# Kernel tuning notes

Hardware: AMD Instinct MI355X
Metric: run time of the kernel (lower is better)

The kernel has to match this reference:

```python
import jax, jax.numpy as jnp
import numpy as np

B, T, C = 4, 2048, 1024
H, HS = 16, 64


def setup_inputs() -> dict:
    key = jax.random.key(0)
    ks = jax.random.split(key, 5)
    scale = (H * C) ** (-0.5)
    x = jax.random.normal(ks[0], (B, T, C), dtype=jnp.float32)
    Wk = jax.random.normal(ks[1], (H, C, HS), dtype=jnp.float32) * scale
    Wq = jax.random.normal(ks[2], (H, C, HS), dtype=jnp.float32) * scale
    Wv = jax.random.normal(ks[3], (H, C, HS), dtype=jnp.float32) * scale
    proj_w = jax.random.normal(ks[4], (C, C), dtype=jnp.float32) / C ** 0.5
    proj_b = jnp.zeros((C,), dtype=jnp.float32)
    return {"x": x, "Wk": Wk, "Wq": Wq, "Wv": Wv, "proj_w": proj_w, "proj_b": proj_b}


def reference(x, Wk, Wq, Wv, proj_w, proj_b):
    b, t, c = x.shape
    # per-head projections: (B,T,C) x (H,C,D) -> (B,H,T,D)
    q = jnp.einsum('btc,hcd->bhtd', x, Wq)
    k = jnp.einsum('btc,hcd->bhtd', x, Wk)
    v = jnp.einsum('btc,hcd->bhtd', x, Wv)
    # NOTE: original module does not scale by 1/sqrt(head_size)
    wei = jnp.einsum('bhtd,bhsd->bhts', q, k)  # (B,H,T,T)
    causal = jnp.tril(jnp.ones((t, t), dtype=bool))
    wei = jnp.where(causal, wei, -jnp.inf)
    wei = jax.nn.softmax(wei, axis=-1)
    out = jnp.einsum('bhts,bhsd->bhtd', wei, v)
    out = out.transpose(0, 2, 1, 3).reshape(b, t, c)  # concat heads
    return out @ proj_w + proj_b
```

## Files before the change

### kernel.cpp

```cpp
#include <hip/hip_runtime.h>

typedef unsigned short u16;
typedef u16 u16x4 __attribute__((ext_vector_type(4)));
typedef u16 u16x8 __attribute__((ext_vector_type(8)));
typedef unsigned uint2v __attribute__((ext_vector_type(2)));
typedef unsigned uint4v __attribute__((ext_vector_type(4)));
typedef __bf16 bf16x2 __attribute__((ext_vector_type(2)));
typedef __bf16 bf16x8 __attribute__((ext_vector_type(8)));
typedef float f32x4 __attribute__((ext_vector_type(4)));

#define DEV static __device__ __forceinline__

DEV u16 f2bf(float f) {
  union { float f; unsigned u; } v; v.f = f;
  return (u16)((v.u + 0x7FFFu + ((v.u >> 16) & 1u)) >> 16);
}

DEV void async16(const void* g, void* l) {
  __builtin_amdgcn_global_load_lds((const __attribute__((address_space(1))) void*)g,
                                   (__attribute__((address_space(3))) void*)l, 16, 0, 0);
}

DEV f32x4 mfma16(bf16x8 a, bf16x8 b, f32x4 c) {
  return __builtin_amdgcn_mfma_f32_16x16x32_bf16(a, b, c, 0, 0, 0);
}

DEV float exp2fast(float x) { return __builtin_amdgcn_exp2f(x); }

#define BARRIER() asm volatile("s_barrier" ::: "memory")
#define SB0() __builtin_amdgcn_sched_barrier(0)

__global__ __launch_bounds__(256) void k_prep(const float* __restrict__ x,
                                              const float* __restrict__ Wk,
                                              const float* __restrict__ Wq,
                                              const float* __restrict__ Wv,
                                              const float* __restrict__ pw,
                                              u16* __restrict__ xb,
                                              u16* __restrict__ wT,
                                              u16* __restrict__ pwT) {
  __shared__ float t[64 * 72];
  const int bid = blockIdx.x, tid = threadIdx.x;
  if (bid < 8192) {
    int i = bid * 1024 + tid * 4;
    float4 v = *(const float4*)(x + i);
    u16x4 o = { f2bf(v.x), f2bf(v.y), f2bf(v.z), f2bf(v.w) };
    *(u16x4*)(xb + i) = o;
    return;
  }
  const int role = bid - 8192;
  const float* src;
  u16* dst;
  int rows, cols, bx, by, bz;
  float scale;
  if (role < 768) {
    const int w = role >> 8, rem = role & 255;
    src = (w == 0) ? Wq : ((w == 1) ? Wk : Wv);
    dst = wT + (size_t)w * 1024 * 1024;
    scale = (w == 0) ? 1.44269504088896340736f : 1.0f;
    rows = 1024; cols = 64; bx = 0; by = rem >> 4; bz = rem & 15;
  } else {
    const int p = role - 768;
    src = pw; dst = pwT; scale = 1.0f;
    rows = 1024; cols = 1024; bx = p & 15; by = p >> 4; bz = 0;
  }
  src += (size_t)bz * rows * cols;
  dst += (size_t)bz * rows * cols;
  const int c0 = bx * 64, r0 = by * 64;
  const int rr = tid >> 2, cb = (tid & 3) * 16;
  const float* s = src + (size_t)(r0 + rr) * cols + c0 + cb;
  float4 v0 = *(const float4*)(s + 0);
  float4 v1 = *(const float4*)(s + 4);
  float4 v2 = *(const float4*)(s + 8);
  float4 v3 = *(const float4*)(s + 12);
  *(float4*)(t + rr * 72 + cb + 0)  = v0;
  *(float4*)(t + rr * 72 + cb + 4)  = v1;
  *(float4*)(t + rr * 72 + cb + 8)  = v2;
  *(float4*)(t + rr * 72 + cb + 12) = v3;
  __syncthreads();
  const int dd = tid >> 2, eb = (tid & 3) * 16;
  u16x8 o0, o1;
#pragma unroll
  for (int e = 0; e < 8; ++e) o0[e] = f2bf(t[(eb + e) * 72 + dd] * scale);
#pragma unroll
  for (int e = 0; e < 8; ++e) o1[e] = f2bf(t[(eb + 8 + e) * 72 + dd] * scale);
  u16* dp = dst + (size_t)(c0 + dd) * rows + r0 + eb;
  *(u16x8*)dp = o0;
  *(u16x8*)(dp + 8) = o1;
}

template <int MODE>
__global__ __launch_bounds__(512, 2) void k_gemm(const u16* __restrict__ A,
                                                 const u16* __restrict__ Bt,
                                                 u16* __restrict__ qd,
                                                 u16* __restrict__ kd,
                                                 u16* __restrict__ vd,
                                                 float* __restrict__ out,
                                                 const float* __restrict__ bias) {
  __shared__ u16 lds[3 * 24576];
  const int tid = threadIdx.x;
  const int w = tid >> 6, lane = tid & 63;
  const int quad = lane >> 4, l15 = lane & 15;
  const int wm = w >> 1, wn = w & 1;

  const int gx = (int)gridDim.x;
  int lin = (int)blockIdx.y * gx + (int)blockIdx.x;
  const int nwg = gx * (int)gridDim.y;
  lin = (lin & 7) * (nwg >> 3) + (lin >> 3);
  const size_t mb = (size_t)(lin / gx);
  const int nb = lin % gx;

  const int lr = lane >> 3;
  const int lc = ((lane & 7) ^ lr) << 3;
  const u16* ga0 = A  + (mb * 256 + (size_t)(w * 8 + lr)) * 1024 + lc;
  const u16* gb0 = Bt + ((size_t)nb * 128 + (size_t)(w * 8 + lr)) * 1024 + lc;

  const int swz0 = ((0 + quad) ^ (l15 & 7)) << 3;
  const int swz1 = ((4 + quad) ^ (l15 & 7)) << 3;

  f32x4 acc[4][4] = {};

#pragma unroll
  for (int s2 = 0; s2 < 2; ++s2) {
    u16* d = lds + s2 * 24576 + w * 512;
#pragma unroll
    for (int g = 0; g < 4; ++g) async16(ga0 + (size_t)g * 65536 + s2 * 64, d + g * 4096);
#pragma unroll
    for (int g = 0; g < 2; ++g) async16(gb0 + (size_t)g * 65536 + s2 * 64, d + 16384 + g * 4096);
  }
  asm volatile("s_waitcnt vmcnt(6)" ::: "memory");
  BARRIER(); SB0();

#pragma unroll
  for (int s = 0; s < 16; ++s) {
    const u16* Ab = lds + (s % 3) * 24576;
    const u16* Bb = Ab + 16384;

    bf16x8 a0[4], b0[4];
#pragma unroll
    for (int i = 0; i < 4; ++i)
      a0[i] = *(const bf16x8*)(Ab + (wm * 64 + i * 16 + l15) * 64 + swz0);
#pragma unroll
    for (int j = 0; j < 4; ++j)
      b0[j] = *(const bf16x8*)(Bb + (wn * 64 + j * 16 + l15) * 64 + swz0);
    if (s < 14) {
      u16* d = lds + ((s + 2) % 3) * 24576 + w * 512;
      async16(ga0 + 0 * 65536 + (s + 2) * 64, d + 0 * 4096);
      async16(ga0 + 1 * 65536 + (s + 2) * 64, d + 1 * 4096);
      async16(ga0 + 2 * 65536 + (s + 2) * 64, d + 2 * 4096);
    }
    SB0(); BARRIER(); SB0();
    __builtin_amdgcn_s_setprio(1);
#pragma unroll
    for (int i = 0; i < 4; ++i)
#pragma unroll
      for (int j = 0; j < 4; ++j) acc[i][j] = mfma16(a0[i], b0[j], acc[i][j]);
    __builtin_amdgcn_s_setprio(0);
    SB0(); BARRIER(); SB0();

    bf16x8 a1[4], b1[4];
#pragma unroll
    for (int i = 0; i < 4; ++i)
      a1[i] = *(const bf16x8*)(Ab + (wm * 64 + i * 16 + l15) * 64 + swz1);
#pragma unroll
    for (int j = 0; j < 4; ++j)
      b1[j] = *(const bf16x8*)(Bb + (wn * 64 + j * 16 + l15) * 64 + swz1);
    if (s < 14) {
      u16* d = lds + ((s + 2) % 3) * 24576 + w * 512;
      async16(ga0 + 3 * 65536 + (s + 2) * 64, d + 3 * 4096);
      async16(gb0 + 0 * 65536 + (s + 2) * 64, d + 16384 + 0 * 4096);
      async16(gb0 + 1 * 65536 + (s + 2) * 64, d + 16384 + 4096);
    }
    SB0(); BARRIER(); SB0();
    __builtin_amdgcn_s_setprio(1);
#pragma unroll
    for (int i = 0; i < 4; ++i)
#pragma unroll
      for (int j = 0; j < 4; ++j) acc[i][j] = mfma16(a1[i], b1[j], acc[i][j]);
    __builtin_amdgcn_s_setprio(0);
    SB0();
    if (s < 14)       { asm volatile("s_waitcnt vmcnt(6)" ::: "memory"); }
    else if (s == 14) { asm volatile("s_waitcnt vmcnt(0)" ::: "memory"); }
    if (s < 15) { BARRIER(); SB0(); }
  }

  const size_t m0 = mb * 256 + wm * 64;
  const int n0 = nb * 128 + wn * 64;
  if (MODE == 0) {
#pragma unroll
    for (int j = 0; j < 4; ++j) {
      const int n = n0 + j * 16 + l15;
      const int p = n >> 10, hh = (n >> 6) & 15, d = n & 63;
      if (p == 2) {
#pragma unroll
        for (int i = 0; i < 4; ++i) {
          const size_t m = m0 + i * 16 + quad * 4;
          const size_t bb = m >> 11, tt = m & 2047;
          u16x4 pk = { f2bf(acc[i][j][0]), f2bf(acc[i][j][1]),
                       f2bf(acc[i][j][2]), f2bf(acc[i][j][3]) };
          *(u16x4*)(vd + ((bb * 16 + hh) * 64 + d) * 2048 + tt) = pk;
        }
      } else {
        u16* dst = (p == 0) ? qd : kd;
#pragma unroll
        for (int i = 0; i < 4; ++i)
#pragma unroll
          for (int r = 0; r < 4; ++r) {
            const size_t m = m0 + i * 16 + quad * 4 + r;
            const size_t bb = m >> 11, tt = m & 2047;
            dst[((bb * 16 + hh) * 2048 + tt) * 64 + d] = f2bf(acc[i][j][r]);
          }
      }
    }
  } else {
#pragma unroll
    for (int j = 0; j < 4; ++j) {
      const int n = n0 + j * 16 + l15;
      const float bv = bias[n];
#pragma unroll
      for (int i = 0; i < 4; ++i)
#pragma unroll
        for (int r = 0; r < 4; ++r) {
          const size_t m = m0 + i * 16 + quad * 4 + r;
          out[m * 1024 + n] = acc[i][j][r] + bv;
        }
    }
  }
}

__global__ __launch_bounds__(256) void k_attn(const u16* __restrict__ Qg,
                                              const u16* __restrict__ Kg,
                                              const u16* __restrict__ Vtg,
                                              u16* __restrict__ Og) {
  __shared__ u16 Kbuf[2 * 4096];
  __shared__ u16 Vbuf[2 * 4096];
  const int tid = threadIdx.x;
  const int wave = tid >> 6, lane = tid & 63;
  const int quad = lane >> 4, l15 = lane & 15;
  const int quad4 = quad * 4, quad8 = quad * 8;
  const int bh = blockIdx.x;
  const int qb = 15 - (int)blockIdx.y;
  const u16* kg = Kg + (size_t)bh * 2048 * 64;
  const u16* vg = Vtg + (size_t)bh * 64 * 2048;
  const int b = bh >> 4, h = bh & 15;

  const int lrow = lane >> 3;
  const int lchunk = ((lane & 7) ^ lrow) << 3;
  const u16* kst = kg + (size_t)(wave * 16 + lrow) * 64 + lchunk;
  const u16* vst = vg + (size_t)(wave * 16 + lrow) * 2048 + lchunk;
  u16* kdst0 = Kbuf + wave * 1024;
  u16* vdst0 = Vbuf + wave * 1024;

  const int rowoff = l15 * 64;
  const int swz0 = ((0 + quad) ^ (l15 & 7)) << 3;
  const int swz1 = ((4 + quad) ^ (l15 & 7)) << 3;

  const int qlo = qb * 128 + wave * 32;
  const int ntw = 2 * qb + 1 + (wave >> 1);
  const int ntb = 2 * qb + 2;
  const u16* qg = Qg + ((size_t)bh * 2048 + (size_t)qb * 128) * 64;

  bf16x8 qf[2][2];
#pragma unroll
  for (int i = 0; i < 2; ++i)
#pragma unroll
    for (int c = 0; c < 2; ++c)
      qf[i][c] = *(const bf16x8*)(qg + (size_t)(wave * 32 + i * 16 + l15) * 64 +
                                  c * 32 + quad8);

  f32x4 oacc[2][4] = {};
  f32x4 lacc[2] = {};
  const f32x4 fzero = {};
  const u16x8 onesu = {0x3F80, 0x3F80, 0x3F80, 0x3F80,
                       0x3F80, 0x3F80, 0x3F80, 0x3F80};
  const bf16x8 onesf = __builtin_bit_cast(bf16x8, onesu);

  async16(kst, kdst0);
  async16(kst + 512, kdst0 + 512);
  async16(vst, vdst0);
  async16(vst + 16384, vdst0 + 512);

  for (int it = 0; it < ntb; ++it) {
    __syncthreads();

    if (it + 1 < ntb) {
      const int buf = (it + 1) & 1;
      const size_t s0n = (size_t)(it + 1) * 64;
      async16(kst + s0n * 64,       kdst0 + buf * 4096);
      async16(kst + s0n * 64 + 512, kdst0 + buf * 4096 + 512);
      async16(vst + s0n,            vdst0 + buf * 4096);
      async16(vst + s0n + 16384,    vdst0 + buf * 4096 + 512);
    }

    if (it < ntw) {
      const int s0 = it * 64;
      const u16* Kb = Kbuf + (it & 1) * 4096;
      const u16* Vb = Vbuf + (it & 1) * 4096;

      f32x4 sacc[4][2];
      __builtin_amdgcn_s_setprio(1);
#pragma unroll
      for (int j = 0; j < 4; ++j) {
        bf16x8 kf0 = *(const bf16x8*)(Kb + j * 1024 + rowoff + swz0);
        bf16x8 kf1 = *(const bf16x8*)(Kb + j * 1024 + rowoff + swz1);
        sacc[j][0] = mfma16(kf0, qf[0][0], fzero);
        sacc[j][0] = mfma16(kf1, qf[0][1], sacc[j][0]);
        sacc[j][1] = mfma16(kf0, qf[1][0], fzero);
        sacc[j][1] = mfma16(kf1, qf[1][1], sacc[j][1]);
      }
      __builtin_amdgcn_s_setprio(0);

#pragma unroll
      for (int j = 0; j < 4; ++j)
#pragma unroll
        for (int i = 0; i < 2; ++i)
#pragma unroll
          for (int r = 0; r < 4; ++r)
            sacc[j][i][r] = exp2fast(sacc[j][i][r]);

      if (it == ntw - 1) {
#pragma unroll
        for (int j = 0; j < 4; ++j)
#pragma unroll
          for (int i = 0; i < 2; ++i)
#pragma unroll
            for (int r = 0; r < 4; ++r)
              if (s0 + j * 16 + quad4 + r > qlo + i * 16 + l15) sacc[j][i][r] = 0.f;
      }

      bf16x8 pa[2][2];
#pragma unroll
      for (int i = 0; i < 2; ++i) {
        unsigned P[8];
#pragma unroll
        for (int j = 0; j < 4; ++j) {
          bf16x2 lo = { (__bf16)sacc[j][i][0], (__bf16)sacc[j][i][1] };
          bf16x2 hi = { (__bf16)sacc[j][i][2], (__bf16)sacc[j][i][3] };
          P[j * 2 + 0] = __builtin_bit_cast(unsigned, lo);
          P[j * 2 + 1] = __builtin_bit_cast(unsigned, hi);
        }
        unsigned wd[8];
#pragma unroll
        for (int g = 0; g < 4; ++g) {
          const int x = (g & 2) * 2 + (g & 1);
          uint2v t = __builtin_amdgcn_permlane32_swap(P[x], P[x + 2], false, false);
          uint2v u = __builtin_amdgcn_permlane16_swap(t.x, t.y, false, false);
          wd[x] = u.x;
          wd[x + 2] = u.y;
        }
        uint4v lo4 = { wd[0], wd[1], wd[2], wd[3] };
        uint4v hi4 = { wd[4], wd[5], wd[6], wd[7] };
        pa[i][0] = __builtin_bit_cast(bf16x8, lo4);
        pa[i][1] = __builtin_bit_cast(bf16x8, hi4);
      }

      __builtin_amdgcn_s_setprio(1);
#pragma unroll
      for (int n = 0; n < 4; ++n) {
        bf16x8 vf0 = *(const bf16x8*)(Vb + n * 1024 + rowoff + swz0);
        bf16x8 vf1 = *(const bf16x8*)(Vb + n * 1024 + rowoff + swz1);
        oacc[0][n] = mfma16(pa[0][0], vf0, oacc[0][n]);
        oacc[0][n] = mfma16(pa[0][1], vf1, oacc[0][n]);
        oacc[1][n] = mfma16(pa[1][0], vf0, oacc[1][n]);
        oacc[1][n] = mfma16(pa[1][1], vf1, oacc[1][n]);
      }
      lacc[0] = mfma16(pa[0][0], onesf, lacc[0]);
      lacc[0] = mfma16(pa[0][1], onesf, lacc[0]);
      lacc[1] = mfma16(pa[1][0], onesf, lacc[1]);
      lacc[1] = mfma16(pa[1][1], onesf, lacc[1]);
      __builtin_amdgcn_s_setprio(0);
    }
  }

#pragma unroll
  for (int i = 0; i < 2; ++i)
#pragma unroll
    for (int r = 0; r < 4; ++r) {
      const float inv = 1.0f / lacc[i][r];
      const size_t t = (size_t)qb * 128 + wave * 32 + i * 16 + quad4 + r;
#pragma unroll
      for (int n = 0; n < 4; ++n)
        Og[((size_t)b * 2048 + t) * 1024 + h * 64 + n * 16 + l15] =
            f2bf(oacc[i][n][r] * inv);
    }
}

extern "C" void kernel_launch(void* const* d_in, const int* in_sizes, int n_in,
                              void* d_out, int out_size, void* d_ws, size_t ws_size,
                              hipStream_t stream) {
  const float* x  = (const float*)d_in[0];
  const float* Wk = (const float*)d_in[1];
  const float* Wq = (const float*)d_in[2];
  const float* Wv = (const float*)d_in[3];
  const float* pw = (const float*)d_in[4];
  const float* pb = (const float*)d_in[5];
  float* out = (float*)d_out;
  char* ws = (char*)d_ws;

  u16* xb  = (u16*)(ws + 0);
  u16* wT  = (u16*)(ws + 16777216);
  u16* pwT = (u16*)(ws + 23068672);
  u16* q   = (u16*)(ws + 25165824);
  u16* kb  = (u16*)(ws + 41943040);
  u16* vt  = (u16*)(ws + 58720256);
  u16* att = (u16*)(ws + 0);

  k_prep<<<9216, 256, 0, stream>>>(x, Wk, Wq, Wv, pw, xb, wT, pwT);
  k_gemm<0><<<dim3(24, 32), 512, 0, stream>>>(xb, wT, q, kb, vt, nullptr, nullptr);
  k_attn<<<dim3(64, 16), 256, 0, stream>>>(q, kb, vt, att);
  k_gemm<1><<<dim3(8, 32), 512, 0, stream>>>(att, pwT, nullptr, nullptr, nullptr, out, pb);
}
```

Measured before the change: 235.1 us.

## Widen QKV GEMM tile to 256 columns and simplify to double-buffered pipeline

```diff
diff --git a/kernel.cpp b/kernel.cpp
--- a/kernel.cpp
+++ b/kernel.cpp
@@ -26,9 +26,6 @@
 }
 
 DEV float exp2fast(float x) { return __builtin_amdgcn_exp2f(x); }
-
-#define BARRIER() asm volatile("s_barrier" ::: "memory")
-#define SB0() __builtin_amdgcn_sched_barrier(0)
 
 __global__ __launch_bounds__(256) void k_prep(const float* __restrict__ x,
                                               const float* __restrict__ Wk,
@@ -96,103 +93,86 @@
                                                  u16* __restrict__ vd,
                                                  float* __restrict__ out,
                                                  const float* __restrict__ bias) {
-  __shared__ u16 lds[3 * 24576];
+  constexpr int BN   = (MODE == 0) ? 256 : 128;
+  constexpr int AI   = (MODE == 0) ? 8 : 4;
+  constexpr int AJ   = 4;
+  constexpr int WN   = (MODE == 0) ? 4 : 2;
+  constexpr int GB   = BN / 64;
+  constexpr int GXC  = (MODE == 0) ? 12 : 8;
+  constexpr int STEPU = (256 + BN) * 64;
+  __shared__ u16 lds[2 * STEPU];
+
   const int tid = threadIdx.x;
   const int w = tid >> 6, lane = tid & 63;
   const int quad = lane >> 4, l15 = lane & 15;
-  const int wm = w >> 1, wn = w & 1;
-
-  const int gx = (int)gridDim.x;
-  int lin = (int)blockIdx.y * gx + (int)blockIdx.x;
-  const int nwg = gx * (int)gridDim.y;
-  lin = (lin & 7) * (nwg >> 3) + (lin >> 3);
-  const size_t mb = (size_t)(lin / gx);
-  const int nb = lin % gx;
+  const int wm = w / WN, wn = w % WN;
+
+  constexpr int NWG = GXC * 32;
+  int lin = (int)blockIdx.y * GXC + (int)blockIdx.x;
+  lin = (lin & 7) * (NWG >> 3) + (lin >> 3);
+  const size_t mb = (size_t)(lin / GXC);
+  const int nb = lin % GXC;
 
   const int lr = lane >> 3;
   const int lc = ((lane & 7) ^ lr) << 3;
   const u16* ga0 = A  + (mb * 256 + (size_t)(w * 8 + lr)) * 1024 + lc;
-  const u16* gb0 = Bt + ((size_t)nb * 128 + (size_t)(w * 8 + lr)) * 1024 + lc;
+  const u16* gb0 = Bt + ((size_t)nb * BN + (size_t)(w * 8 + lr)) * 1024 + lc;
 
   const int swz0 = ((0 + quad) ^ (l15 & 7)) << 3;
   const int swz1 = ((4 + quad) ^ (l15 & 7)) << 3;
 
-  f32x4 acc[4][4] = {};
-
-#pragma unroll
-  for (int s2 = 0; s2 < 2; ++s2) {
-    u16* d = lds + s2 * 24576 + w * 512;
-#pragma unroll
-    for (int g = 0; g < 4; ++g) async16(ga0 + (size_t)g * 65536 + s2 * 64, d + g * 4096);
-#pragma unroll
-    for (int g = 0; g < 2; ++g) async16(gb0 + (size_t)g * 65536 + s2 * 64, d + 16384 + g * 4096);
-  }
-  asm volatile("s_waitcnt vmcnt(6)" ::: "memory");
-  BARRIER(); SB0();
-
-#pragma unroll
+  f32x4 acc[AI][AJ] = {};
+
+  auto STAGE = [&](int buf, int s) {
+    u16* sb = lds + buf * STEPU + w * 512;
+    const int ko = s * 64;
+#pragma unroll
+    for (int g = 0; g < 4; ++g)
+      async16(ga0 + (size_t)g * 65536 + ko, sb + g * 4096);
+#pragma unroll
+    for (int g = 0; g < GB; ++g)
+      async16(gb0 + (size_t)g * 65536 + ko, sb + 16384 + g * 4096);
+  };
+
+  STAGE(0, 0);
+  __syncthreads();
+
   for (int s = 0; s < 16; ++s) {
-    const u16* Ab = lds + (s % 3) * 24576;
+    const int buf = s & 1;
+    if (s < 15) STAGE(buf ^ 1, s + 1);
+    const u16* Ab = lds + buf * STEPU;
     const u16* Bb = Ab + 16384;
 
-    bf16x8 a0[4], b0[4];
-#pragma unroll
-    for (int i = 0; i < 4; ++i)
-      a0[i] = *(const bf16x8*)(Ab + (wm * 64 + i * 16 + l15) * 64 + swz0);
-#pragma unroll
-    for (int j = 0; j < 4; ++j)
-      b0[j] = *(const bf16x8*)(Bb + (wn * 64 + j * 16 + l15) * 64 + swz0);
-    if (s < 14) {
-      u16* d = lds + ((s + 2) % 3) * 24576 + w * 512;
-      async16(ga0 + 0 * 65536 + (s + 2) * 64, d + 0 * 4096);
-      async16(ga0 + 1 * 65536 + (s + 2) * 64, d + 1 * 4096);
-      async16(ga0 + 2 * 65536 + (s + 2) * 64, d + 2 * 4096);
-    }
-    SB0(); BARRIER(); SB0();
-    __builtin_amdgcn_s_setprio(1);
-#pragma unroll
-    for (int i = 0; i < 4; ++i)
-#pragma unroll
-      for (int j = 0; j < 4; ++j) acc[i][j] = mfma16(a0[i], b0[j], acc[i][j]);
-    __builtin_amdgcn_s_setprio(0);
-    SB0(); BARRIER(); SB0();
-
-    bf16x8 a1[4], b1[4];
-#pragma unroll
-    for (int i = 0; i < 4; ++i)
-      a1[i] = *(const bf16x8*)(Ab + (wm * 64 + i * 16 + l15) * 64 + swz1);
-#pragma unroll
-    for (int j = 0; j < 4; ++j)
-      b1[j] = *(const bf16x8*)(Bb + (wn * 64 + j * 16 + l15) * 64 + swz1);
-    if (s < 14) {
-      u16* d = lds + ((s + 2) % 3) * 24576 + w * 512;
-      async16(ga0 + 3 * 65536 + (s + 2) * 64, d + 3 * 4096);
-      async16(gb0 + 0 * 65536 + (s + 2) * 64, d + 16384 + 0 * 4096);
-      async16(gb0 + 1 * 65536 + (s + 2) * 64, d + 16384 + 4096);
-    }
-    SB0(); BARRIER(); SB0();
-    __builtin_amdgcn_s_setprio(1);
-#pragma unroll
-    for (int i = 0; i < 4; ++i)
-#pragma unroll
-      for (int j = 0; j < 4; ++j) acc[i][j] = mfma16(a1[i], b1[j], acc[i][j]);
-    __builtin_amdgcn_s_setprio(0);
-    SB0();
-    if (s < 14)       { asm volatile("s_waitcnt vmcnt(6)" ::: "memory"); }
-    else if (s == 14) { asm volatile("s_waitcnt vmcnt(0)" ::: "memory"); }
-    if (s < 15) { BARRIER(); SB0(); }
-  }
-
-  const size_t m0 = mb * 256 + wm * 64;
-  const int n0 = nb * 128 + wn * 64;
+#pragma unroll
+    for (int c = 0; c < 2; ++c) {
+      const int swz = c ? swz1 : swz0;
+      bf16x8 af[AI], bf[AJ];
+#pragma unroll
+      for (int i = 0; i < AI; ++i)
+        af[i] = *(const bf16x8*)(Ab + (wm * (AI * 16) + i * 16 + l15) * 64 + swz);
+#pragma unroll
+      for (int j = 0; j < AJ; ++j)
+        bf[j] = *(const bf16x8*)(Bb + (wn * (AJ * 16) + j * 16 + l15) * 64 + swz);
+      __builtin_amdgcn_s_setprio(1);
+#pragma unroll
+      for (int i = 0; i < AI; ++i)
+#pragma unroll
+        for (int j = 0; j < AJ; ++j) acc[i][j] = mfma16(af[i], bf[j], acc[i][j]);
+      __builtin_amdgcn_s_setprio(0);
+    }
+    __syncthreads();
+  }
+
+  const size_t m0 = mb * 256 + wm * (AI * 16);
+  const int n0 = nb * BN + wn * (AJ * 16);
   if (MODE == 0) {
 #pragma unroll
-    for (int j = 0; j < 4; ++j) {
+    for (int j = 0; j < AJ; ++j) {
       const int n = n0 + j * 16 + l15;
       const int p = n >> 10, hh = (n >> 6) & 15, d = n & 63;
       if (p == 2) {
 #pragma unroll
-        for (int i = 0; i < 4; ++i) {
+        for (int i = 0; i < AI; ++i) {
           const size_t m = m0 + i * 16 + quad * 4;
           const size_t bb = m >> 11, tt = m & 2047;
           u16x4 pk = { f2bf(acc[i][j][0]), f2bf(acc[i][j][1]),
@@ -202,7 +182,7 @@
       } else {
         u16* dst = (p == 0) ? qd : kd;
 #pragma unroll
-        for (int i = 0; i < 4; ++i)
+        for (int i = 0; i < AI; ++i)
 #pragma unroll
           for (int r = 0; r < 4; ++r) {
             const size_t m = m0 + i * 16 + quad * 4 + r;
@@ -213,11 +193,11 @@
     }
   } else {
 #pragma unroll
-    for (int j = 0; j < 4; ++j) {
+    for (int j = 0; j < AJ; ++j) {
       const int n = n0 + j * 16 + l15;
       const float bv = bias[n];
 #pragma unroll
-      for (int i = 0; i < 4; ++i)
+      for (int i = 0; i < AI; ++i)
 #pragma unroll
         for (int r = 0; r < 4; ++r) {
           const size_t m = m0 + i * 16 + quad * 4 + r;
@@ -321,10 +301,10 @@
 #pragma unroll
         for (int j = 0; j < 4; ++j)
 #pragma unroll
-          for (int i = 0; i < 2; ++i)
-#pragma unroll
-            for (int r = 0; r < 4; ++r)
-              if (s0 + j * 16 + quad4 + r > qlo + i * 16 + l15) sacc[j][i][r] = 0.f;
+        for (int i = 0; i < 2; ++i)
+#pragma unroll
+          for (int r = 0; r < 4; ++r)
+            if (s0 + j * 16 + quad4 + r > qlo + i * 16 + l15) sacc[j][i][r] = 0.f;
       }
 
       bf16x8 pa[2][2];
@@ -405,7 +385,7 @@
   u16* att = (u16*)(ws + 0);
 
   k_prep<<<9216, 256, 0, stream>>>(x, Wk, Wq, Wv, pw, xb, wT, pwT);
-  k_gemm<0><<<dim3(24, 32), 512, 0, stream>>>(xb, wT, q, kb, vt, nullptr, nullptr);
+  k_gemm<0><<<dim3(12, 32), 512, 0, stream>>>(xb, wT, q, kb, vt, nullptr, nullptr);
   k_attn<<<dim3(64, 16), 256, 0, stream>>>(q, kb, vt, att);
   k_gemm<1><<<dim3(8, 32), 512, 0, stream>>>(att, pwT, nullptr, nullptr, nullptr, out, pb);
 }
```

Measured after the change: 241.7 us. 2.8% more time.

## Simplify GEMM main loop to one barrier per K-step with hoisted LDS reads

Applied to the files above, without the earlier changes.

```diff
diff --git a/kernel.cpp b/kernel.cpp
--- a/kernel.cpp
+++ b/kernel.cpp
@@ -96,18 +96,18 @@
                                                  u16* __restrict__ vd,
                                                  float* __restrict__ out,
                                                  const float* __restrict__ bias) {
+  constexpr int GXC = (MODE == 0) ? 24 : 8;
   __shared__ u16 lds[3 * 24576];
   const int tid = threadIdx.x;
   const int w = tid >> 6, lane = tid & 63;
   const int quad = lane >> 4, l15 = lane & 15;
   const int wm = w >> 1, wn = w & 1;
 
-  const int gx = (int)gridDim.x;
-  int lin = (int)blockIdx.y * gx + (int)blockIdx.x;
-  const int nwg = gx * (int)gridDim.y;
-  lin = (lin & 7) * (nwg >> 3) + (lin >> 3);
-  const size_t mb = (size_t)(lin / gx);
-  const int nb = lin % gx;
+  constexpr int NWG = GXC * 32;
+  int lin = (int)blockIdx.y * GXC + (int)blockIdx.x;
+  lin = (lin & 7) * (NWG >> 3) + (lin >> 3);
+  const size_t mb = (size_t)(lin / GXC);
+  const int nb = lin % GXC;
 
   const int lr = lane >> 3;
   const int lc = ((lane & 7) ^ lr) << 3;
@@ -119,68 +119,57 @@
 
   f32x4 acc[4][4] = {};
 
-#pragma unroll
-  for (int s2 = 0; s2 < 2; ++s2) {
-    u16* d = lds + s2 * 24576 + w * 512;
-#pragma unroll
-    for (int g = 0; g < 4; ++g) async16(ga0 + (size_t)g * 65536 + s2 * 64, d + g * 4096);
-#pragma unroll
-    for (int g = 0; g < 2; ++g) async16(gb0 + (size_t)g * 65536 + s2 * 64, d + 16384 + g * 4096);
-  }
+  auto STAGE = [&](int buf, int s) {
+    u16* sb = lds + buf * 24576 + w * 512;
+    const int ko = s * 64;
+#pragma unroll
+    for (int g = 0; g < 4; ++g)
+      async16(ga0 + (size_t)g * 65536 + ko, sb + g * 4096);
+#pragma unroll
+    for (int g = 0; g < 2; ++g)
+      async16(gb0 + (size_t)g * 65536 + ko, sb + 16384 + g * 4096);
+  };
+
+  STAGE(0, 0);
+  STAGE(1, 1);
   asm volatile("s_waitcnt vmcnt(6)" ::: "memory");
   BARRIER(); SB0();
 
-#pragma unroll
   for (int s = 0; s < 16; ++s) {
     const u16* Ab = lds + (s % 3) * 24576;
     const u16* Bb = Ab + 16384;
-
-    bf16x8 a0[4], b0[4];
+    if (s < 14) STAGE((s + 2) % 3, s + 2);
+
+    bf16x8 a0[4], b0[4], a1[4], b1[4];
+#pragma unroll
+    for (int i = 0; i < 4; ++i) {
+      a0[i] = *(const bf16x8*)(Ab + (wm * 64 + i * 16 + l15) * 64 + swz0);
+      a1[i] = *(const bf16x8*)(Ab + (wm * 64 + i * 16 + l15) * 64 + swz1);
+    }
+#pragma unroll
+    for (int j = 0; j < 4; ++j) {
+      b0[j] = *(const bf16x8*)(Bb + (wn * 64 + j * 16 + l15) * 64 + swz0);
+      b1[j] = *(const bf16x8*)(Bb + (wn * 64 + j * 16 + l15) * 64 + swz1);
+    }
+    __builtin_amdgcn_s_setprio(1);
 #pragma unroll
     for (int i = 0; i < 4; ++i)
-      a0[i] = *(const bf16x8*)(Ab + (wm * 64 + i * 16 + l15) * 64 + swz0);
-#pragma unroll
-    for (int j = 0; j < 4; ++j)
-      b0[j] = *(const bf16x8*)(Bb + (wn * 64 + j * 16 + l15) * 64 + swz0);
-    if (s < 14) {
-      u16* d = lds + ((s + 2) % 3) * 24576 + w * 512;
-      async16(ga0 + 0 * 65536 + (s + 2) * 64, d + 0 * 4096);
-      async16(ga0 + 1 * 65536 + (s + 2) * 64, d + 1 * 4096);
-      async16(ga0 + 2 * 65536 + (s + 2) * 64, d + 2 * 4096);
-    }
-    SB0(); BARRIER(); SB0();
-    __builtin_amdgcn_s_setprio(1);
-#pragma unroll
-    for (int i = 0; i < 4; ++i)
 #pragma unroll
       for (int j = 0; j < 4; ++j) acc[i][j] = mfma16(a0[i], b0[j], acc[i][j]);
-    __builtin_amdgcn_s_setprio(0);
-    SB0(); BARRIER(); SB0();
-
-    bf16x8 a1[4], b1[4];
-#pragma unroll
-    for (int i = 0; i < 4; ++i)
-      a1[i] = *(const bf16x8*)(Ab + (wm * 64 + i * 16 + l15) * 64 + swz1);
-#pragma unroll
-    for (int j = 0; j < 4; ++j)
-      b1[j] = *(const bf16x8*)(Bb + (wn * 64 + j * 16 + l15) * 64 + swz1);
-    if (s < 14) {
-      u16* d = lds + ((s + 2) % 3) * 24576 + w * 512;
-      async16(ga0 + 3 * 65536 + (s + 2) * 64, d + 3 * 4096);
-      async16(gb0 + 0 * 65536 + (s + 2) * 64, d + 16384 + 0 * 4096);
-      async16(gb0 + 1 * 65536 + (s + 2) * 64, d + 16384 + 4096);
-    }
-    SB0(); BARRIER(); SB0();
-    __builtin_amdgcn_s_setprio(1);
 #pragma unroll
     for (int i = 0; i < 4; ++i)
 #pragma unroll
       for (int j = 0; j < 4; ++j) acc[i][j] = mfma16(a1[i], b1[j], acc[i][j]);
     __builtin_amdgcn_s_setprio(0);
+
     SB0();
-    if (s < 14)       { asm volatile("s_waitcnt vmcnt(6)" ::: "memory"); }
-    else if (s == 14) { asm volatile("s_waitcnt vmcnt(0)" ::: "memory"); }
-    if (s < 15) { BARRIER(); SB0(); }
+    if (s < 14) {
+      asm volatile("s_waitcnt vmcnt(6) lgkmcnt(0)" ::: "memory");
+      BARRIER(); SB0();
+    } else if (s == 14) {
+      asm volatile("s_waitcnt vmcnt(0) lgkmcnt(0)" ::: "memory");
+      BARRIER(); SB0();
+    }
   }
 
   const size_t m0 = mb * 256 + wm * 64;
@@ -321,10 +310,10 @@
 #pragma unroll
         for (int j = 0; j < 4; ++j)
 #pragma unroll
-          for (int i = 0; i < 2; ++i)
-#pragma unroll
-            for (int r = 0; r < 4; ++r)
-              if (s0 + j * 16 + quad4 + r > qlo + i * 16 + l15) sacc[j][i][r] = 0.f;
+        for (int i = 0; i < 2; ++i)
+#pragma unroll
+          for (int r = 0; r < 4; ++r)
+            if (s0 + j * 16 + quad4 + r > qlo + i * 16 + l15) sacc[j][i][r] = 0.f;
       }
 
       bf16x8 pa[2][2];
```

Measured after the change: 239.5 us. No clear change (+1.9%).
